# Kernel optimization log

Hardware: AMD Instinct MI355X
Metric: run time of the kernel (lower is better)

## Reference

```python
import jax, jax.numpy as jnp
import numpy as np

D_MODEL = 1024
NUM_HEADS = 16
D_K = D_MODEL // NUM_HEADS
SIM_THRESH = 0.7


def setup_inputs() -> dict:
    key = jax.random.key(0)
    ks = jax.random.split(key, 7)
    bs, seq = 2, 2048
    scale = 1.0 / np.sqrt(D_MODEL)
    x = jax.random.normal(ks[0], (bs, seq, D_MODEL), dtype=jnp.float32)
    Wq = jax.random.normal(ks[1], (D_MODEL, D_MODEL), dtype=jnp.float32) * scale
    Wk = jax.random.normal(ks[2], (D_MODEL, D_MODEL), dtype=jnp.float32) * scale
    Wv = jax.random.normal(ks[3], (D_MODEL, D_MODEL), dtype=jnp.float32) * scale
    bq = jax.random.normal(ks[4], (D_MODEL,), dtype=jnp.float32) * scale
    bk = jax.random.normal(ks[5], (D_MODEL,), dtype=jnp.float32) * scale
    bv = jax.random.normal(ks[6], (D_MODEL,), dtype=jnp.float32) * scale
    return {"x": x, "Wq": Wq, "bq": bq, "Wk": Wk, "bk": bk, "Wv": Wv, "bv": bv}


def reference(x, Wq, bq, Wk, bk, Wv, bv):
    bs, seq, d_model = x.shape
    # dynamic structural mask: cosine similarity > 0.7, shared across heads
    norm_x = x / jnp.maximum(jnp.linalg.norm(x, axis=-1, keepdims=True), 1e-12)
    sim = jnp.einsum('bsd,btd->bst', norm_x, norm_x)          # [B,S,S]
    mask = (sim > SIM_THRESH)[:, None, :, :]                  # [B,1,S,S]

    def proj(W, b):
        y = x @ W.T + b                                        # [B,S,D]
        return y.reshape(bs, seq, NUM_HEADS, D_K).transpose(0, 2, 1, 3)  # [B,H,S,dk]

    q = proj(Wq, bq)
    k = proj(Wk, bk)
    v = proj(Wv, bv)

    scores = jnp.einsum('bhsd,bhtd->bhst', q, k) / jnp.sqrt(jnp.float32(D_K))
    scores = jnp.where(mask, scores, -jnp.inf)
    attn = jax.nn.softmax(scores, axis=-1)                     # diag always unmasked
    return jnp.einsum('bhst,bhtd->bhsd', attn, v)              # [B,H,S,dk]
```

## Files before the change

kernel.cpp:

```cpp
#include <hip/hip_runtime.h>
#include <stdint.h>
#include <math.h>

#define D_MODEL 1024
#define NUM_HEADS 16
#define D_K 64
#define SEQ 2048
#define BATCH 2
#define SIM_THRESH 0.7f

#define BM 128
#define BN 128
#define BK 32

#define NROWS (BATCH * SEQ)
#define VP_BLOCKS ((NROWS / BM) * (D_MODEL / BN))
#define SIM_TRI 136
#define SIM_BLOCKS (SIM_TRI * BATCH)

typedef __attribute__((ext_vector_type(8))) short bf16x8;
typedef __attribute__((ext_vector_type(4))) float f32x4;

static __device__ __forceinline__ unsigned short f2bf(float f) {
    unsigned int u = __float_as_uint(f);
    unsigned int r = (u + 0x7FFF + ((u >> 16) & 1)) >> 16;
    return (unsigned short)r;
}
static __device__ __forceinline__ float bf2f(unsigned short u) {
    return __uint_as_float(((unsigned int)u) << 16);
}

__global__ __launch_bounds__(256) void k_prep(const float* __restrict__ x,
                                              const float* __restrict__ Wv,
                                              unsigned short* __restrict__ xn,
                                              unsigned short* __restrict__ Wvb,
                                              float* __restrict__ norms,
                                              int* __restrict__ cnt) {
    int bid = blockIdx.x, tid = threadIdx.x;
    if (bid < NROWS) {
        const float4* xr = (const float4*)(x + (size_t)bid * D_MODEL);
        float4 vv = xr[tid];
        float ss = vv.x * vv.x + vv.y * vv.y + vv.z * vv.z + vv.w * vv.w;
        for (int off = 32; off > 0; off >>= 1) ss += __shfl_down(ss, off, 64);
        __shared__ float wsum[4];
        int lane = tid & 63, wv = tid >> 6;
        if (lane == 0) wsum[wv] = ss;
        __syncthreads();
        float nrm = sqrtf(wsum[0] + wsum[1] + wsum[2] + wsum[3]);
        float inv = 1.0f / fmaxf(nrm, 1e-12f);
        ushort4 o;
        o.x = f2bf(vv.x * inv); o.y = f2bf(vv.y * inv);
        o.z = f2bf(vv.z * inv); o.w = f2bf(vv.w * inv);
        *(ushort4*)(xn + (size_t)bid * D_MODEL + tid * 4) = o;
        if (tid == 0) { norms[bid] = nrm; cnt[bid] = 0; }
    } else {
        size_t i = (size_t)(bid - NROWS) * 256 + tid;
        float4 w = ((const float4*)Wv)[i];
        ushort4 o;
        o.x = f2bf(w.x); o.y = f2bf(w.y); o.z = f2bf(w.z); o.w = f2bf(w.w);
        *(ushort4*)(Wvb + i * 4) = o;
    }
}

static __device__ __forceinline__ void stage_tile(const unsigned short* __restrict__ gsrc,
                                                  int rowBase, int kk,
                                                  short* ldsDst, int tid) {
#pragma unroll
    for (int p = 0; p < 2; ++p) {
        int idx = p * 256 + tid;
        int row = idx >> 2;
        int ch  = idx & 3;
        const unsigned short* ga = gsrc + (size_t)(rowBase + row) * D_MODEL + kk + ch * 8;
        __builtin_amdgcn_global_load_lds(
            (const __attribute__((address_space(1))) unsigned int*)ga,
            (__attribute__((address_space(3))) unsigned int*)(ldsDst + idx * 8),
            16, 0, 0);
    }
}

__global__ __launch_bounds__(256) void k_main(const unsigned short* __restrict__ xn,
                                              const unsigned short* __restrict__ Wvb,
                                              const float* __restrict__ bv,
                                              const float* __restrict__ norms,
                                              float* __restrict__ v,
                                              int* __restrict__ cnt,
                                              float* __restrict__ out) {
    __shared__ short As[BM * BK];
    __shared__ short Bs[BN * BK];
    int bid = blockIdx.x;
    int tid = threadIdx.x;
    int lane = tid & 63, wave = tid >> 6;
    int wm = wave & 1, wn = wave >> 1;
    int lrow = lane & 15, quad = lane >> 4;

    const unsigned short* Asrc;
    const unsigned short* Bsrc;
    int rowBase, colBase;
    bool isV;
    int b = 0, bi = 0, bj = 0;
    if (bid < VP_BLOCKS) {
        isV = true;
        rowBase = (bid >> 3) * BM;
        colBase = (bid & 7) * BN;
        Asrc = xn;
        Bsrc = Wvb;
    } else {
        isV = false;
        int sidx = bid - VP_BLOCKS;
        b = (sidx >= SIM_TRI) ? 1 : 0;
        int idx = sidx - b * SIM_TRI;
        int r = idx;
        bi = 0;
        while (r >= 16 - bi) { r -= 16 - bi; ++bi; }
        bj = bi + r;
        rowBase = bi * BM;
        colBase = bj * BN;
        Asrc = xn + (size_t)b * SEQ * D_MODEL;
        Bsrc = Asrc;
    }

    int aoff[4], boff[4];
#pragma unroll
    for (int i = 0; i < 4; ++i) {
        aoff[i] = (wm * 64 + i * 16 + lrow) * BK + quad * 8;
        boff[i] = (wn * 64 + i * 16 + lrow) * BK + quad * 8;
    }
    f32x4 acc[4][4] = {};
    for (int kk = 0; kk < D_MODEL; kk += BK) {
        stage_tile(Asrc, rowBase, kk, As, tid);
        stage_tile(Bsrc, colBase, kk, Bs, tid);
        __syncthreads();
        bf16x8 av[4], bvv[4];
#pragma unroll
        for (int i = 0; i < 4; ++i) av[i] = *(const bf16x8*)(As + aoff[i]);
#pragma unroll
        for (int i = 0; i < 4; ++i) bvv[i] = *(const bf16x8*)(Bs + boff[i]);
#pragma unroll
        for (int mt = 0; mt < 4; ++mt)
#pragma unroll
            for (int nt = 0; nt < 4; ++nt)
                acc[mt][nt] = __builtin_amdgcn_mfma_f32_16x16x32_bf16(av[mt], bvv[nt], acc[mt][nt], 0, 0, 0);
        __syncthreads();
    }

    if (isV) {
#pragma unroll
        for (int mt = 0; mt < 4; ++mt) {
#pragma unroll
            for (int nt = 0; nt < 4; ++nt) {
                int n = colBase + wn * 64 + nt * 16 + lrow;
                float bn = bv[n];
                int h = n >> 6, j = n & 63;
#pragma unroll
                for (int r = 0; r < 4; ++r) {
                    int m = rowBase + wm * 64 + mt * 16 + quad * 4 + r;
                    float val = acc[mt][nt][r] * norms[m] + bn;
                    v[(size_t)m * D_MODEL + n] = val;
                    int bb = m >> 11, s = m & (SEQ - 1);
                    out[(((size_t)(bb * NUM_HEADS + h)) * SEQ + s) * D_K + j] = val;
                }
            }
        }
    } else {
        int* cb = cnt + b * SEQ;
        bool diag = (bi == bj);
#pragma unroll
        for (int mt = 0; mt < 4; ++mt) {
#pragma unroll
            for (int nt = 0; nt < 4; ++nt) {
                int n = colBase + wn * 64 + nt * 16 + lrow;
#pragma unroll
                for (int r = 0; r < 4; ++r) {
                    int m = rowBase + wm * 64 + mt * 16 + quad * 4 + r;
                    if (acc[mt][nt][r] > SIM_THRESH) {
                        atomicAdd(&cb[m], 1);
                        if (!diag) atomicAdd(&cb[n], 1);
                    }
                }
            }
        }
    }
}

__global__ __launch_bounds__(256) void k_fix(
    const float* __restrict__ x,
    const float* __restrict__ Wq, const float* __restrict__ bq,
    const float* __restrict__ Wk, const float* __restrict__ bk,
    const float* __restrict__ v,
    const unsigned short* __restrict__ xn,
    const int* __restrict__ cnt,
    float* __restrict__ out)
{
    int tid = threadIdx.x;
    int rowBase = blockIdx.x * 256;

    __shared__ int list[256];
    __shared__ int nlist;
    if (tid == 0) nlist = 0;
    __syncthreads();
    int grow = rowBase + tid;
    if (cnt[grow] != 1) { int p = atomicAdd(&nlist, 1); list[p] = grow; }
    __syncthreads();
    int nfix = nlist;
    if (nfix == 0) return;

    __shared__ uint8_t mrow[SEQ];
    __shared__ float q_row[D_MODEL];
    __shared__ float k_row[D_MODEL];
    __shared__ float accO[D_MODEL];
    __shared__ float m_h[NUM_HEADS], l_h[NUM_HEADS], alpha_h[NUM_HEADS], p_h[NUM_HEADS];

    for (int li = 0; li < nfix; ++li) {
        int row = list[li];
        int b = row >> 11, s = row & (SEQ - 1);

        const unsigned short* xs = xn + (size_t)row * D_MODEL;
        for (int t = tid; t < SEQ; t += 256) {
            const unsigned short* xt = xn + ((size_t)b * SEQ + t) * D_MODEL;
            float d = 0.f;
            for (int k = 0; k < D_MODEL; ++k) d += bf2f(xs[k]) * bf2f(xt[k]);
            mrow[t] = (d > SIM_THRESH) ? 1 : 0;
        }

        const float* xrow = x + (size_t)row * D_MODEL;
        for (int c = tid; c < D_MODEL; c += 256) {
            const float* w = Wq + (size_t)c * D_MODEL;
            float acc = bq[c];
            for (int d = 0; d < D_MODEL; ++d) acc += xrow[d] * w[d];
            q_row[c] = acc;
            accO[c] = 0.f;
        }
        if (tid < NUM_HEADS) { m_h[tid] = -INFINITY; l_h[tid] = 0.f; }
        __syncthreads();

        for (int t = 0; t < SEQ; ++t) {
            if (!mrow[t]) continue;
            const float* xt = x + ((size_t)b * SEQ + t) * D_MODEL;
            for (int c = tid; c < D_MODEL; c += 256) {
                const float* w = Wk + (size_t)c * D_MODEL;
                float acc = bk[c];
                for (int d = 0; d < D_MODEL; ++d) acc += xt[d] * w[d];
                k_row[c] = acc;
            }
            __syncthreads();
            if (tid < NUM_HEADS) {
                float sc = 0.f;
                for (int j = 0; j < D_K; ++j) sc += q_row[tid * D_K + j] * k_row[tid * D_K + j];
                sc *= 0.125f;
                float mnew = fmaxf(m_h[tid], sc);
                float alpha = expf(m_h[tid] - mnew);
                float p = expf(sc - mnew);
                l_h[tid] = l_h[tid] * alpha + p;
                m_h[tid] = mnew;
                alpha_h[tid] = alpha;
                p_h[tid] = p;
            }
            __syncthreads();
            const float* vt = v + ((size_t)b * SEQ + t) * D_MODEL;
            for (int c = tid; c < D_MODEL; c += 256) {
                int h = c >> 6;
                accO[c] = accO[c] * alpha_h[h] + p_h[h] * vt[c];
            }
            __syncthreads();
        }
        for (int c = tid; c < D_MODEL; c += 256) {
            int h = c >> 6, j = c & 63;
            out[(((size_t)(b * NUM_HEADS + h)) * SEQ + s) * D_K + j] = accO[c] / l_h[h];
        }
        __syncthreads();
    }
}

extern "C" void kernel_launch(void* const* d_in, const int* in_sizes, int n_in,
                              void* d_out, int out_size, void* d_ws, size_t ws_size,
                              hipStream_t stream) {
    const float* x  = (const float*)d_in[0];
    const float* Wq = (const float*)d_in[1];
    const float* bq = (const float*)d_in[2];
    const float* Wk = (const float*)d_in[3];
    const float* bk = (const float*)d_in[4];
    const float* Wv = (const float*)d_in[5];
    const float* bv = (const float*)d_in[6];
    float* out = (float*)d_out;

    unsigned short* xn  = (unsigned short*)d_ws;
    unsigned short* Wvb = xn + (size_t)NROWS * D_MODEL;
    float* v     = (float*)(Wvb + (size_t)D_MODEL * D_MODEL);
    float* norms = v + (size_t)NROWS * D_MODEL;
    int* cnt     = (int*)(norms + NROWS);

    k_prep<<<NROWS + D_MODEL * D_MODEL / 1024, 256, 0, stream>>>(x, Wv, xn, Wvb, norms, cnt);

    k_main<<<VP_BLOCKS + SIM_BLOCKS, 256, 0, stream>>>(xn, Wvb, bv, norms, v, cnt, out);

    k_fix<<<NROWS / 256, 256, 0, stream>>>(x, Wq, bq, Wk, bk, v, xn, cnt, out);
}
```

Before: 130.8 us.

## Shrink GEMM tiles to 64x64 with BK=64 and double-buffered LDS staging

Reduces the k_main output tile from 128x128 to 64x64, doubles the K step to 64, and adds double-buffered LDS so the next tile's global_load_lds is issued before computing on the current one. The block count goes from about 528 to about 2080, which spreads work more evenly across the mi355x compute units and leaves one barrier per iteration instead of two. The cost is lower data reuse per block: more global and LDS traffic per MFMA and fewer MFMAs per LDS read.

```diff
diff --git a/kernel.cpp b/kernel.cpp
--- a/kernel.cpp
+++ b/kernel.cpp
@@ -9,14 +9,18 @@
 #define BATCH 2
 #define SIM_THRESH 0.7f
 
-#define BM 128
-#define BN 128
-#define BK 32
+#define TS 64
+#define BK 64
+#define NIT (D_MODEL / BK)
 
 #define NROWS (BATCH * SEQ)
-#define VP_BLOCKS ((NROWS / BM) * (D_MODEL / BN))
-#define SIM_TRI 136
+#define VP_BLOCKS ((NROWS / TS) * (D_MODEL / TS))
+#define SIM_ROWB (SEQ / TS)
+#define SIM_TRI (SIM_ROWB * (SIM_ROWB + 1) / 2)
 #define SIM_BLOCKS (SIM_TRI * BATCH)
+#define GRID (VP_BLOCKS + SIM_BLOCKS)
+
+#define TILE_SH (TS * BK)
 
 typedef __attribute__((ext_vector_type(8))) short bf16x8;
 typedef __attribute__((ext_vector_type(4))) float f32x4;
@@ -62,14 +66,14 @@
     }
 }
 
-static __device__ __forceinline__ void stage_tile(const unsigned short* __restrict__ gsrc,
-                                                  int rowBase, int kk,
-                                                  short* ldsDst, int tid) {
+static __device__ __forceinline__ void stage64(const unsigned short* __restrict__ gsrc,
+                                               int rowBase, int kk,
+                                               short* ldsDst, int tid) {
 #pragma unroll
     for (int p = 0; p < 2; ++p) {
         int idx = p * 256 + tid;
-        int row = idx >> 2;
-        int ch  = idx & 3;
+        int row = idx >> 3;
+        int ch  = idx & 7;
         const unsigned short* ga = gsrc + (size_t)(rowBase + row) * D_MODEL + kk + ch * 8;
         __builtin_amdgcn_global_load_lds(
             (const __attribute__((address_space(1))) unsigned int*)ga,
@@ -85,8 +89,8 @@
                                               float* __restrict__ v,
                                               int* __restrict__ cnt,
                                               float* __restrict__ out) {
-    __shared__ short As[BM * BK];
-    __shared__ short Bs[BN * BK];
+    __shared__ short As[2 * TILE_SH];
+    __shared__ short Bs[2 * TILE_SH];
     int bid = blockIdx.x;
     int tid = threadIdx.x;
     int lane = tid & 63, wave = tid >> 6;
@@ -100,60 +104,70 @@
     int b = 0, bi = 0, bj = 0;
     if (bid < VP_BLOCKS) {
         isV = true;
-        rowBase = (bid >> 3) * BM;
-        colBase = (bid & 7) * BN;
+        rowBase = (bid >> 4) * TS;
+        colBase = (bid & 15) * TS;
         Asrc = xn;
         Bsrc = Wvb;
     } else {
         isV = false;
         int sidx = bid - VP_BLOCKS;
         b = (sidx >= SIM_TRI) ? 1 : 0;
-        int idx = sidx - b * SIM_TRI;
-        int r = idx;
+        int r = sidx - b * SIM_TRI;
         bi = 0;
-        while (r >= 16 - bi) { r -= 16 - bi; ++bi; }
+        while (r >= SIM_ROWB - bi) { r -= SIM_ROWB - bi; ++bi; }
         bj = bi + r;
-        rowBase = bi * BM;
-        colBase = bj * BN;
+        rowBase = bi * TS;
+        colBase = bj * TS;
         Asrc = xn + (size_t)b * SEQ * D_MODEL;
         Bsrc = Asrc;
     }
 
-    int aoff[4], boff[4];
-#pragma unroll
-    for (int i = 0; i < 4; ++i) {
-        aoff[i] = (wm * 64 + i * 16 + lrow) * BK + quad * 8;
-        boff[i] = (wn * 64 + i * 16 + lrow) * BK + quad * 8;
-    }
-    f32x4 acc[4][4] = {};
-    for (int kk = 0; kk < D_MODEL; kk += BK) {
-        stage_tile(Asrc, rowBase, kk, As, tid);
-        stage_tile(Bsrc, colBase, kk, Bs, tid);
+    int aoff[2], boff[2];
+#pragma unroll
+    for (int i = 0; i < 2; ++i) {
+        aoff[i] = (wm * 32 + i * 16 + lrow) * BK + quad * 8;
+        boff[i] = (wn * 32 + i * 16 + lrow) * BK + quad * 8;
+    }
+    f32x4 acc[2][2] = {};
+
+    stage64(Asrc, rowBase, 0, As, tid);
+    stage64(Bsrc, colBase, 0, Bs, tid);
+    __syncthreads();
+    for (int it = 0; it < NIT; ++it) {
+        int cur = it & 1, nxt = cur ^ 1;
+        if (it + 1 < NIT) {
+            stage64(Asrc, rowBase, (it + 1) * BK, As + nxt * TILE_SH, tid);
+            stage64(Bsrc, colBase, (it + 1) * BK, Bs + nxt * TILE_SH, tid);
+        }
+        const short* Ac = As + cur * TILE_SH;
+        const short* Bc = Bs + cur * TILE_SH;
+#pragma unroll
+        for (int kb = 0; kb < 2; ++kb) {
+            bf16x8 av[2], bvv[2];
+#pragma unroll
+            for (int i = 0; i < 2; ++i) av[i]  = *(const bf16x8*)(Ac + aoff[i] + kb * 32);
+#pragma unroll
+            for (int i = 0; i < 2; ++i) bvv[i] = *(const bf16x8*)(Bc + boff[i] + kb * 32);
+#pragma unroll
+            for (int mt = 0; mt < 2; ++mt)
+#pragma unroll
+                for (int nt = 0; nt < 2; ++nt)
+                    acc[mt][nt] = __builtin_amdgcn_mfma_f32_16x16x32_bf16(av[mt], bvv[nt], acc[mt][nt], 0, 0, 0);
+        }
         __syncthreads();
-        bf16x8 av[4], bvv[4];
-#pragma unroll
-        for (int i = 0; i < 4; ++i) av[i] = *(const bf16x8*)(As + aoff[i]);
-#pragma unroll
-        for (int i = 0; i < 4; ++i) bvv[i] = *(const bf16x8*)(Bs + boff[i]);
-#pragma unroll
-        for (int mt = 0; mt < 4; ++mt)
-#pragma unroll
-            for (int nt = 0; nt < 4; ++nt)
-                acc[mt][nt] = __builtin_amdgcn_mfma_f32_16x16x32_bf16(av[mt], bvv[nt], acc[mt][nt], 0, 0, 0);
-        __syncthreads();
     }
 
     if (isV) {
 #pragma unroll
-        for (int mt = 0; mt < 4; ++mt) {
-#pragma unroll
-            for (int nt = 0; nt < 4; ++nt) {
-                int n = colBase + wn * 64 + nt * 16 + lrow;
+        for (int mt = 0; mt < 2; ++mt) {
+#pragma unroll
+            for (int nt = 0; nt < 2; ++nt) {
+                int n = colBase + wn * 32 + nt * 16 + lrow;
                 float bn = bv[n];
                 int h = n >> 6, j = n & 63;
 #pragma unroll
                 for (int r = 0; r < 4; ++r) {
-                    int m = rowBase + wm * 64 + mt * 16 + quad * 4 + r;
+                    int m = rowBase + wm * 32 + mt * 16 + quad * 4 + r;
                     float val = acc[mt][nt][r] * norms[m] + bn;
                     v[(size_t)m * D_MODEL + n] = val;
                     int bb = m >> 11, s = m & (SEQ - 1);
@@ -165,13 +179,13 @@
         int* cb = cnt + b * SEQ;
         bool diag = (bi == bj);
 #pragma unroll
-        for (int mt = 0; mt < 4; ++mt) {
-#pragma unroll
-            for (int nt = 0; nt < 4; ++nt) {
-                int n = colBase + wn * 64 + nt * 16 + lrow;
+        for (int mt = 0; mt < 2; ++mt) {
+#pragma unroll
+            for (int nt = 0; nt < 2; ++nt) {
+                int n = colBase + wn * 32 + nt * 16 + lrow;
 #pragma unroll
                 for (int r = 0; r < 4; ++r) {
-                    int m = rowBase + wm * 64 + mt * 16 + quad * 4 + r;
+                    int m = rowBase + wm * 32 + mt * 16 + quad * 4 + r;
                     if (acc[mt][nt][r] > SIM_THRESH) {
                         atomicAdd(&cb[m], 1);
                         if (!diag) atomicAdd(&cb[n], 1);
@@ -291,7 +305,7 @@
 
     k_prep<<<NROWS + D_MODEL * D_MODEL / 1024, 256, 0, stream>>>(x, Wv, xn, Wvb, norms, cnt);
 
-    k_main<<<VP_BLOCKS + SIM_BLOCKS, 256, 0, stream>>>(xn, Wvb, bv, norms, v, cnt, out);
+    k_main<<<GRID, 256, 0, stream>>>(xn, Wvb, bv, norms, v, cnt, out);
 
     k_fix<<<NROWS / 256, 256, 0, stream>>>(x, Wq, bq, Wk, bk, v, xn, cnt, out);
 }
```

After: 135.3 us. 1.03x slower.
